# Optimization experiments

Measured on AMD Instinct MI355X. Metric: run time of the kernel, lower is better.

## Reference

```python
import jax, jax.numpy as jnp
import numpy as np

N_NODES = 100000
N_EDGES = 1200000
D_IN = 64
H1 = 64
H2 = 64
N_CLASSES = 40
K_HOPS = 3  # PyG TAGConv default K=3


def _gcn_norm(edge_index, num_nodes):
    # TAGConv uses gcn_norm WITHOUT adding self-loops.
    src, dst = edge_index[0], edge_index[1]
    ones = jnp.ones((src.shape[0],), dtype=jnp.float32)
    deg = jax.ops.segment_sum(ones, dst, num_segments=num_nodes)
    deg_inv_sqrt = jnp.where(deg > 0, jax.lax.rsqrt(jnp.maximum(deg, 1.0)), 0.0)
    return deg_inv_sqrt[src] * deg_inv_sqrt[dst]  # [E]


def _tag_conv(x, src, dst, norm, W, b, num_nodes, K):
    # out = concat([x, Ax, ..., A^K x]) @ W + b, A = D^-1/2 A D^-1/2
    hops = [x]
    h = x
    for _ in range(K):
        h = jax.ops.segment_sum(h[src] * norm[:, None], dst, num_segments=num_nodes)
        hops.append(h)
    return jnp.concatenate(hops, axis=-1) @ W + b


def setup_inputs() -> dict:
    key = jax.random.key(0)
    ks = jax.random.split(key, 9)
    x = jax.random.normal(ks[0], (N_NODES, D_IN), dtype=jnp.float32)
    edge_index = jax.random.randint(ks[1], (2, N_EDGES), 0, N_NODES, dtype=jnp.int64)
    W1 = jax.random.normal(ks[2], ((K_HOPS + 1) * D_IN, H1), dtype=jnp.float32) * 0.05
    b1 = jnp.zeros((H1,), dtype=jnp.float32)
    W2 = jax.random.normal(ks[3], ((K_HOPS + 1) * H1, H2), dtype=jnp.float32) * 0.05
    b2 = jnp.zeros((H2,), dtype=jnp.float32)
    Wc = jax.random.normal(ks[4], (H2, N_CLASSES), dtype=jnp.float32) * 0.05
    bc = jnp.zeros((N_CLASSES,), dtype=jnp.float32)
    return {"x": x, "edge_index": edge_index, "W1": W1, "b1": b1,
            "W2": W2, "b2": b2, "Wc": Wc, "bc": bc}


def reference(x, edge_index, W1, b1, W2, b2, Wc, bc):
    num_nodes = x.shape[0]
    src, dst = edge_index[0], edge_index[1]
    norm = _gcn_norm(edge_index, num_nodes)
    h = _tag_conv(x, src, dst, norm, W1, b1, num_nodes, K_HOPS)
    h = jax.nn.relu(h)  # dropout is identity at inference
    h = _tag_conv(h, src, dst, norm, W2, b2, num_nodes, K_HOPS)
    h = jax.nn.relu(h)
    return h @ Wc + bc  # [N, num_classes]
```

## Files before the change

### kernel.cpp

```cpp
#include <hip/hip_runtime.h>
#include <hip/hip_bf16.h>
#include <stdint.h>

static constexpr int TG_NN = 100000;
static constexpr int TG_NE = 1200000;
static constexpr int TG_D  = 64;
static constexpr int TG_NC = 40;
static constexpr int TG_BT = 256;
static constexpr int TG_GN = (TG_NN + TG_BT - 1) / TG_BT;
static constexpr int TG_CAP = 64;
static constexpr int TG_WSH = 15;
static constexpr int TG_NPASS = (TG_NN + (1 << TG_WSH) - 1) >> TG_WSH;
static constexpr int TG_NR = TG_NN + 128;
static constexpr long TG_BS = (long)TG_NR * TG_D;

typedef __attribute__((ext_vector_type(8))) short tg71_s8;
typedef __attribute__((ext_vector_type(4))) float tg71_f4;

__device__ __forceinline__ float tg71_b2f(unsigned short u) {
    return __uint_as_float(((unsigned int)u) << 16);
}
__device__ __forceinline__ unsigned short tg71_f2b(float v) {
    __hip_bfloat16 b = __float2bfloat16(v);
    return __builtin_bit_cast(unsigned short, b);
}
__device__ __forceinline__ float tg71_ld(const void* p, long i, int isF32) {
    if (isF32) return ((const float*)p)[i];
    return tg71_b2f(((const unsigned short*)p)[i]);
}
__device__ __forceinline__ void tg71_st(void* p, long i, int isF32, float v) {
    if (isF32) ((float*)p)[i] = v;
    else ((unsigned short*)p)[i] = tg71_f2b(v);
}
__device__ __forceinline__ float4 tg71_u2f4(ushort4 u) {
    return float4{tg71_b2f(u.x), tg71_b2f(u.y), tg71_b2f(u.z), tg71_b2f(u.w)};
}

__global__ void tg71_detect(const int* ei, const unsigned short* w1bits, int* flags) {
    int lane = threadIdx.x;
    int hi = ei[2 * lane + 1];
    unsigned long long bi = __ballot(hi != 0);
    float mx = 0.0f;
    for (int k = lane; k < 2048; k += 64) {
        float v = fabsf(tg71_b2f(w1bits[k]));
        if (!(v == v)) v = 1e30f;
        mx = fmaxf(mx, v);
    }
    unsigned long long bf = __ballot(mx > 1e4f);
    if (lane == 0) { flags[0] = (bi == 0ULL) ? 1 : 0; flags[1] = (bf != 0ULL) ? 1 : 0; }
}

extern "C" __global__ void TAGModel_71227737636876_kernel(void* out, const int* flags) {
    long i = (long)blockIdx.x * blockDim.x + threadIdx.x;
    if (i < (long)TG_NN * TG_NC) tg71_st(out, i, flags[1], 123.0f);
}

__global__ void tg71_prep(const void* W1, const void* W2, const int* flags,
                          unsigned short* Wt1, unsigned short* Wt2, int* cnt,
                          unsigned short* Sall) {
    int b = blockIdx.x;
    if (b < 128) {
        const void* W = (b < 64) ? W1 : W2;
        unsigned short* Wt = (b < 64) ? Wt1 : Wt2;
        int i = (b & 63) * TG_BT + threadIdx.x;
        int k = i >> 6, n = i & 63;
        Wt[n * 256 + k] = flags[1] ? tg71_f2b(((const float*)W)[i]) : ((const unsigned short*)W)[i];
    } else if (b < 128 + TG_GN) {
        int i = (b - 128) * TG_BT + threadIdx.x;
        if (i < TG_NN) cnt[i] = 0;
    } else {
        int j = (b - 128 - TG_GN) * TG_BT + threadIdx.x;
        if (j < 5 * 2048) {
            int buf = j >> 11, w = j & 2047;
            unsigned short* base = Sall + (long)buf * TG_BS + (long)TG_NN * TG_D;
            ((uint2*)base)[w] = uint2{0u, 0u};
        }
    }
}

__global__ void tg71_scatter(const int* __restrict__ ei, const int* flags,
                             int* __restrict__ srcI, int* __restrict__ dstI,
                             int* cnt, int* __restrict__ srcS, int pass, int decode) {
    int e = blockIdx.x * blockDim.x + threadIdx.x;
    if (e >= TG_NE) return;
    int s, d;
    if (decode) {
        if (flags[0]) { s = ((const int2*)ei)[e].x; d = ((const int2*)ei)[TG_NE + e].x; }
        else          { s = ei[e]; d = ei[TG_NE + e]; }
        srcI[e] = s;
        dstI[e] = d;
    } else {
        s = srcI[e];
        d = dstI[e];
    }
    if ((d >> TG_WSH) != pass) return;
    int pos = atomicAdd(cnt + d, 1);
    if (pos < TG_CAP) srcS[(d << 6) + pos] = s;
}

__global__ void tg71_gx(const void* x, const int* flags, const int* __restrict__ cnt,
                        float* __restrict__ dis, unsigned short* __restrict__ g) {
    int tid = blockIdx.x * blockDim.x + threadIdx.x;
    if (tid >= TG_NN * 4) return;
    int n = tid >> 2, q = tid & 3;
    if (q == 0) {
        int c = cnt[n];
        dis[n] = c > 0 ? rsqrtf((float)c) : 0.f;
    }
    unsigned short* dst = g + (long)n * TG_D + q * 16;
    if (flags[1]) {
        const float* p = (const float*)x + (long)n * TG_D + q * 16;
        float4 v0 = *(const float4*)p, v1 = *(const float4*)(p + 4);
        float4 v2 = *(const float4*)(p + 8), v3 = *(const float4*)(p + 12);
        tg71_s8 o0, o1;
        o0[0] = (short)tg71_f2b(v0.x); o0[1] = (short)tg71_f2b(v0.y);
        o0[2] = (short)tg71_f2b(v0.z); o0[3] = (short)tg71_f2b(v0.w);
        o0[4] = (short)tg71_f2b(v1.x); o0[5] = (short)tg71_f2b(v1.y);
        o0[6] = (short)tg71_f2b(v1.z); o0[7] = (short)tg71_f2b(v1.w);
        o1[0] = (short)tg71_f2b(v2.x); o1[1] = (short)tg71_f2b(v2.y);
        o1[2] = (short)tg71_f2b(v2.z); o1[3] = (short)tg71_f2b(v2.w);
        o1[4] = (short)tg71_f2b(v3.x); o1[5] = (short)tg71_f2b(v3.y);
        o1[6] = (short)tg71_f2b(v3.z); o1[7] = (short)tg71_f2b(v3.w);
        *(tg71_s8*)dst = o0;
        *(tg71_s8*)(dst + 8) = o1;
    } else {
        const unsigned short* p = (const unsigned short*)x + (long)n * TG_D + q * 16;
        *(tg71_s8*)dst = *(const tg71_s8*)p;
        *(tg71_s8*)(dst + 8) = *(const tg71_s8*)(p + 8);
    }
}

__global__ void tg71_prop(const int* __restrict__ cnt, const int* __restrict__ srcS,
                          const float* __restrict__ dis,
                          const unsigned short* __restrict__ in,
                          unsigned short* __restrict__ out) {
    int gid = blockIdx.x * blockDim.x + threadIdx.x;
    int wid = gid >> 6, lane = gid & 63;
    int grp = lane >> 3, li = lane & 7;
    int n = wid * 8 + grp;
    int len = min(cnt[n], TG_CAP);
    int r0 = n << 6;
    long fo = (long)li * 8;

    int4 qa = *(const int4*)&srcS[r0];
    int4 qb = *(const int4*)&srcS[r0 + 4];
    int4 qc = *(const int4*)&srcS[r0 + 8];
    int4 qd = *(const int4*)&srcS[r0 + 12];
    int idx[16] = {qa.x, qa.y, qa.z, qa.w, qb.x, qb.y, qb.z, qb.w,
                   qc.x, qc.y, qc.z, qc.w, qd.x, qd.y, qd.z, qd.w};

    tg71_s8 w[16];
    float wgt[16];
#pragma unroll
    for (int j = 0; j < 16; ++j) {
        int aj = (j < len) ? idx[j] : 0;
        w[j] = *(const tg71_s8*)&in[(long)aj * TG_D + fo];
        wgt[j] = (j < len) ? dis[aj] : 0.f;
    }

    float acc[8];
#pragma unroll
    for (int f = 0; f < 8; ++f) acc[f] = 0.f;
#pragma unroll
    for (int j = 0; j < 16; ++j) {
#pragma unroll
        for (int f = 0; f < 8; ++f)
            acc[f] += wgt[j] * tg71_b2f((unsigned short)w[j][f]);
    }

    for (int k = 16; k < len; k += 8) {
        int4 ra = *(const int4*)&srcS[r0 + k];
        int4 rb = *(const int4*)&srcS[r0 + k + 4];
        int jdx[8] = {ra.x, ra.y, ra.z, ra.w, rb.x, rb.y, rb.z, rb.w};
        tg71_s8 v[8];
        float vw[8];
#pragma unroll
        for (int j = 0; j < 8; ++j) {
            int aj = (k + j < len) ? jdx[j] : 0;
            v[j] = *(const tg71_s8*)&in[(long)aj * TG_D + fo];
            vw[j] = (k + j < len) ? dis[aj] : 0.f;
        }
#pragma unroll
        for (int j = 0; j < 8; ++j) {
#pragma unroll
            for (int f = 0; f < 8; ++f)
                acc[f] += vw[j] * tg71_b2f((unsigned short)v[j][f]);
        }
    }

    float dn = dis[n];
    tg71_s8 oh;
#pragma unroll
    for (int f = 0; f < 8; ++f) oh[f] = (short)tg71_f2b(acc[f] * dn);
    __builtin_nontemporal_store(oh, (tg71_s8*)&out[(long)n * TG_D + fo]);
}

__global__ __launch_bounds__(256) void tg71_gemm(
    const unsigned short* A0, const unsigned short* A1, const unsigned short* A2,
    const unsigned short* A3, const unsigned short* Wt, const void* bias, const int* flags,
    unsigned short* yOut, int doHead, const void* Wc, const void* bc, void* outp) {
    __shared__ __align__(16) unsigned short sZ[128 * 68];
    __shared__ unsigned short sWc[41 * 68];

    const int t    = threadIdx.x;
    const int wave = t >> 6;
    const int lane = t & 63;
    const int quad = lane >> 4;
    const int lr   = lane & 15;
    const int fF   = flags[1];
    const long tile = (long)blockIdx.x * 128;
    const long row0 = tile + wave * 32 + lr;
    const long row1 = row0 + 16;

    const unsigned short* As[4] = {A0, A1, A2, A3};

    tg71_s8 af[4][2][2];
#pragma unroll
    for (int seg = 0; seg < 4; ++seg)
#pragma unroll
        for (int ks = 0; ks < 2; ++ks)
#pragma unroll
            for (int m = 0; m < 2; ++m)
                af[seg][ks][m] = *(const tg71_s8*)(As[seg] + (m ? row1 : row0) * TG_D +
                                                   ks * 32 + quad * 8);

    tg71_f4 acc[2][4];
#pragma unroll
    for (int mt = 0; mt < 2; ++mt)
#pragma unroll
        for (int nt = 0; nt < 4; ++nt) acc[mt][nt] = tg71_f4{0.f, 0.f, 0.f, 0.f};

#pragma unroll
    for (int seg = 0; seg < 4; ++seg)
#pragma unroll
        for (int ks = 0; ks < 2; ++ks) {
            const int kw = seg * 64 + ks * 32 + quad * 8;
            tg71_s8 b0 = *(const tg71_s8*)&Wt[(0  + lr) * 256 + kw];
            tg71_s8 b1 = *(const tg71_s8*)&Wt[(16 + lr) * 256 + kw];
            tg71_s8 b2 = *(const tg71_s8*)&Wt[(32 + lr) * 256 + kw];
            tg71_s8 b3 = *(const tg71_s8*)&Wt[(48 + lr) * 256 + kw];
            const tg71_s8 a0 = af[seg][ks][0];
            const tg71_s8 a1 = af[seg][ks][1];
            acc[0][0] = __builtin_amdgcn_mfma_f32_16x16x32_bf16(a0, b0, acc[0][0], 0, 0, 0);
            acc[0][1] = __builtin_amdgcn_mfma_f32_16x16x32_bf16(a0, b1, acc[0][1], 0, 0, 0);
            acc[0][2] = __builtin_amdgcn_mfma_f32_16x16x32_bf16(a0, b2, acc[0][2], 0, 0, 0);
            acc[0][3] = __builtin_amdgcn_mfma_f32_16x16x32_bf16(a0, b3, acc[0][3], 0, 0, 0);
            acc[1][0] = __builtin_amdgcn_mfma_f32_16x16x32_bf16(a1, b0, acc[1][0], 0, 0, 0);
            acc[1][1] = __builtin_amdgcn_mfma_f32_16x16x32_bf16(a1, b1, acc[1][1], 0, 0, 0);
            acc[1][2] = __builtin_amdgcn_mfma_f32_16x16x32_bf16(a1, b2, acc[1][2], 0, 0, 0);
            acc[1][3] = __builtin_amdgcn_mfma_f32_16x16x32_bf16(a1, b3, acc[1][3], 0, 0, 0);
        }

    float bv[4];
#pragma unroll
    for (int nt = 0; nt < 4; ++nt) bv[nt] = tg71_ld(bias, nt * 16 + lr, fF);

#pragma unroll
    for (int mt = 0; mt < 2; ++mt) {
#pragma unroll
        for (int r = 0; r < 4; ++r) {
            int ml = wave * 32 + mt * 16 + quad * 4 + r;
#pragma unroll
            for (int nt = 0; nt < 4; ++nt) {
                float v = fmaxf(acc[mt][nt][r] + bv[nt], 0.f);
                sZ[ml * 68 + nt * 16 + lr] = tg71_f2b(v);
            }
        }
    }

    if (!doHead) {
        __syncthreads();
        for (int c = t; c < 2048; c += 256) {
            int m = c >> 4, f4 = (c & 15) * 4;
            *(ushort4*)&yOut[(tile + m) * TG_D + f4] = *(const ushort4*)&sZ[m * 68 + f4];
        }
        return;
    }

    for (int i = t; i < 64 * TG_NC; i += 256) {
        int f = i / TG_NC, c = i - f * TG_NC;
        sWc[c * 68 + f] = fF ? tg71_f2b(((const float*)Wc)[i]) : ((const unsigned short*)Wc)[i];
    }
    if (t < TG_NC) sWc[40 * 68 + t] = fF ? tg71_f2b(((const float*)bc)[t]) : ((const unsigned short*)bc)[t];
    __syncthreads();

    const int jb = t & 7;
    const int mb = t >> 3;
    float hacc[4][5];
#pragma unroll
    for (int i = 0; i < 4; ++i)
#pragma unroll
        for (int q = 0; q < 5; ++q) hacc[i][q] = 0.f;
    for (int fc = 0; fc < 64; fc += 4) {
        float4 zv[4], wv[5];
#pragma unroll
        for (int i = 0; i < 4; ++i)
            zv[i] = tg71_u2f4(*(const ushort4*)&sZ[(mb + 32 * i) * 68 + fc]);
#pragma unroll
        for (int q = 0; q < 5; ++q)
            wv[q] = tg71_u2f4(*(const ushort4*)&sWc[(jb * 5 + q) * 68 + fc]);
#pragma unroll
        for (int i = 0; i < 4; ++i)
#pragma unroll
            for (int q = 0; q < 5; ++q)
                hacc[i][q] += zv[i].x * wv[q].x + zv[i].y * wv[q].y +
                              zv[i].z * wv[q].z + zv[i].w * wv[q].w;
    }
#pragma unroll
    for (int i = 0; i < 4; ++i) {
        long n = tile + mb + 32 * i;
        if (n < TG_NN) {
#pragma unroll
            for (int q = 0; q < 5; ++q) {
                int c = jb * 5 + q;
                tg71_st(outp, n * TG_NC + c, fF, hacc[i][q] + tg71_b2f(sWc[40 * 68 + c]));
            }
        }
    }
}

extern "C" void kernel_launch(void* const* d_in, const int* in_sizes, int n_in,
                              void* d_out, int out_size, void* d_ws, size_t ws_size,
                              hipStream_t stream) {
    const void* x  = d_in[0];
    const int*  ei = (const int*)d_in[1];
    const void* W1 = d_in[2];
    const void* b1 = d_in[3];
    const void* W2 = d_in[4];
    const void* b2 = d_in[5];
    const void* Wc = d_in[6];
    const void* bc = d_in[7];

    int*   flags = (int*)d_ws;
    int*   srcI  = flags + 16;
    int*   dstI  = srcI + TG_NE;
    int*   cnt   = dstI + TG_NE;
    float* dis   = (float*)(cnt + TG_NN);
    int*   srcS  = (int*)(dis + TG_NN);
    unsigned short* Sall = (unsigned short*)(((uintptr_t)(srcS + TG_NN * TG_CAP) + 255) &
                                             ~(uintptr_t)255);
    unsigned short* S1 = Sall + 0 * TG_BS;
    unsigned short* S2 = Sall + 1 * TG_BS;
    unsigned short* S3 = Sall + 2 * TG_BS;
    unsigned short* S4 = Sall + 3 * TG_BS;
    unsigned short* S5 = Sall + 4 * TG_BS;
    unsigned short* Wt1 = Sall + 5 * TG_BS;
    unsigned short* Wt2 = Wt1 + 64 * 256;

    const int gE = (TG_NE + TG_BT - 1) / TG_BT;
    const int gP = TG_NN / 32;
    const int gX = (TG_NN * 4 + TG_BT - 1) / TG_BT;
    const int gT = (TG_NN + 127) / 128;

    tg71_detect<<<1, 64, 0, stream>>>(ei, (const unsigned short*)W1, flags);
    tg71_prep<<<128 + TG_GN + 40, TG_BT, 0, stream>>>(W1, W2, flags, Wt1, Wt2, cnt, Sall);

    for (int pass = 0; pass < TG_NPASS; ++pass)
        tg71_scatter<<<gE, TG_BT, 0, stream>>>(ei, flags, srcI, dstI, cnt, srcS,
                                               pass, pass == 0 ? 1 : 0);

    tg71_gx<<<gX, TG_BT, 0, stream>>>(x, flags, cnt, dis, S1);
    tg71_prop<<<gP, TG_BT, 0, stream>>>(cnt, srcS, dis, S1, S2);
    tg71_prop<<<gP, TG_BT, 0, stream>>>(cnt, srcS, dis, S2, S3);
    tg71_prop<<<gP, TG_BT, 0, stream>>>(cnt, srcS, dis, S3, S4);
    tg71_gemm<<<gT, TG_BT, 0, stream>>>(S1, S2, S3, S4, Wt1, b1, flags,
                                        S5, 0, nullptr, nullptr, nullptr);

    tg71_prop<<<gP, TG_BT, 0, stream>>>(cnt, srcS, dis, S5, S2);
    tg71_prop<<<gP, TG_BT, 0, stream>>>(cnt, srcS, dis, S2, S3);
    tg71_prop<<<gP, TG_BT, 0, stream>>>(cnt, srcS, dis, S3, S4);
    tg71_gemm<<<gT, TG_BT, 0, stream>>>(S5, S2, S3, S4, Wt2, b2, flags,
                                        nullptr, 1, Wc, bc, d_out);
}
```

Baseline: 400.6 us.

## Bucket edges by destination window before CSR scatter instead of multi-pass filtering

```diff
diff --git a/kernel.cpp b/kernel.cpp
--- a/kernel.cpp
+++ b/kernel.cpp
@@ -10,7 +10,8 @@
 static constexpr int TG_GN = (TG_NN + TG_BT - 1) / TG_BT;
 static constexpr int TG_CAP = 64;
 static constexpr int TG_WSH = 15;
-static constexpr int TG_NPASS = (TG_NN + (1 << TG_WSH) - 1) >> TG_WSH;
+static constexpr int TG_CB  = 458752;
+static constexpr int TG_CB3 = 65536;
 static constexpr int TG_NR = TG_NN + 128;
 static constexpr long TG_BS = (long)TG_NR * TG_D;
 
@@ -57,7 +58,7 @@
 
 __global__ void tg71_prep(const void* W1, const void* W2, const int* flags,
                           unsigned short* Wt1, unsigned short* Wt2, int* cnt,
-                          unsigned short* Sall) {
+                          int* bcnt, unsigned short* Sall) {
     int b = blockIdx.x;
     if (b < 128) {
         const void* W = (b < 64) ? W1 : W2;
@@ -68,6 +69,7 @@
     } else if (b < 128 + TG_GN) {
         int i = (b - 128) * TG_BT + threadIdx.x;
         if (i < TG_NN) cnt[i] = 0;
+        if (b == 128 && threadIdx.x < 4) bcnt[threadIdx.x] = 0;
     } else {
         int j = (b - 128 - TG_GN) * TG_BT + threadIdx.x;
         if (j < 5 * 2048) {
@@ -78,24 +80,40 @@
     }
 }
 
-__global__ void tg71_scatter(const int* __restrict__ ei, const int* flags,
-                             int* __restrict__ srcI, int* __restrict__ dstI,
-                             int* cnt, int* __restrict__ srcS, int pass, int decode) {
+__global__ void tg71_bucket(const int* __restrict__ ei, const int* flags,
+                            int2* __restrict__ buck, int* bcnt) {
     int e = blockIdx.x * blockDim.x + threadIdx.x;
     if (e >= TG_NE) return;
     int s, d;
-    if (decode) {
-        if (flags[0]) { s = ((const int2*)ei)[e].x; d = ((const int2*)ei)[TG_NE + e].x; }
-        else          { s = ei[e]; d = ei[TG_NE + e]; }
-        srcI[e] = s;
-        dstI[e] = d;
-    } else {
-        s = srcI[e];
-        d = dstI[e];
-    }
-    if ((d >> TG_WSH) != pass) return;
-    int pos = atomicAdd(cnt + d, 1);
-    if (pos < TG_CAP) srcS[(d << 6) + pos] = s;
+    if (flags[0]) { s = ((const int2*)ei)[e].x; d = ((const int2*)ei)[TG_NE + e].x; }
+    else          { s = ei[e]; d = ei[TG_NE + e]; }
+    int wd = d >> TG_WSH;
+    int lane = threadIdx.x & 63;
+#pragma unroll
+    for (int w = 0; w < 4; ++w) {
+        unsigned long long mw = __ballot(wd == w);
+        if (wd == w) {
+            int leader = __ffsll(mw) - 1;
+            int base = 0;
+            if (lane == leader) base = atomicAdd(bcnt + w, __popcll(mw));
+            base = __shfl(base, leader);
+            int pos = base + (int)__popcll(mw & ((1ull << lane) - 1ull));
+            int cap = (w < 3) ? TG_CB : TG_CB3;
+            if (pos < cap) buck[w * TG_CB + pos] = int2{s, d};
+        }
+    }
+}
+
+__global__ void tg71_scatw(const int2* __restrict__ buck, const int* __restrict__ bcnt,
+                           int* cnt, int* __restrict__ srcS, int w) {
+    int i = blockIdx.x * blockDim.x + threadIdx.x;
+    int n = bcnt[w];
+    int cap = (w < 3) ? TG_CB : TG_CB3;
+    if (n > cap) n = cap;
+    if (i >= n) return;
+    int2 e = buck[w * TG_CB + i];
+    int pos = atomicAdd(cnt + e.y, 1);
+    if (pos < TG_CAP) srcS[(e.y << 6) + pos] = e.x;
 }
 
 __global__ void tg71_gx(const void* x, const int* flags, const int* __restrict__ cnt,
@@ -192,7 +210,7 @@
     tg71_s8 oh;
 #pragma unroll
     for (int f = 0; f < 8; ++f) oh[f] = (short)tg71_f2b(acc[f] * dn);
-    __builtin_nontemporal_store(oh, (tg71_s8*)&out[(long)n * TG_D + fo]);
+    *(tg71_s8*)&out[(long)n * TG_D + fo] = oh;
 }
 
 __global__ __launch_bounds__(256) void tg71_gemm(
@@ -332,9 +350,9 @@
     const void* bc = d_in[7];
 
     int*   flags = (int*)d_ws;
-    int*   srcI  = flags + 16;
-    int*   dstI  = srcI + TG_NE;
-    int*   cnt   = dstI + TG_NE;
+    int*   bcnt  = flags + 8;
+    int2*  buck  = (int2*)(flags + 16);
+    int*   cnt   = (int*)(buck + 3 * TG_CB + TG_CB3);
     float* dis   = (float*)(cnt + TG_NN);
     int*   srcS  = (int*)(dis + TG_NN);
     unsigned short* Sall = (unsigned short*)(((uintptr_t)(srcS + TG_NN * TG_CAP) + 255) &
@@ -351,13 +369,15 @@
     const int gP = TG_NN / 32;
     const int gX = (TG_NN * 4 + TG_BT - 1) / TG_BT;
     const int gT = (TG_NN + 127) / 128;
+    const int gW = TG_CB / TG_BT;
+    const int gW3 = TG_CB3 / TG_BT;
 
     tg71_detect<<<1, 64, 0, stream>>>(ei, (const unsigned short*)W1, flags);
-    tg71_prep<<<128 + TG_GN + 40, TG_BT, 0, stream>>>(W1, W2, flags, Wt1, Wt2, cnt, Sall);
-
-    for (int pass = 0; pass < TG_NPASS; ++pass)
-        tg71_scatter<<<gE, TG_BT, 0, stream>>>(ei, flags, srcI, dstI, cnt, srcS,
-                                               pass, pass == 0 ? 1 : 0);
+    tg71_prep<<<128 + TG_GN + 40, TG_BT, 0, stream>>>(W1, W2, flags, Wt1, Wt2, cnt, bcnt, Sall);
+
+    tg71_bucket<<<gE, TG_BT, 0, stream>>>(ei, flags, buck, bcnt);
+    for (int w = 0; w < 4; ++w)
+        tg71_scatw<<<(w < 3) ? gW : gW3, TG_BT, 0, stream>>>(buck, bcnt, cnt, srcS, w);
 
     tg71_gx<<<gX, TG_BT, 0, stream>>>(x, flags, cnt, dis, S1);
     tg71_prop<<<gP, TG_BT, 0, stream>>>(cnt, srcS, dis, S1, S2);
```

Result: slower. 1.167 ms (+191.3%).
